# Performance work log

Hardware: AMD Instinct MI355X
Metric: run time of the kernel (lower is better)

The kernel has to match this reference:

```python
import jax, jax.numpy as jnp
import numpy as np

H, ND, RD, VD = 16, 128, 64, 128  # heads, nope/rope/v head dims
EPS = 1e-6


def rmsnorm(x, g):
    return x * jax.lax.rsqrt(jnp.mean(x * x, axis=-1, keepdims=True) + EPS) * g


def apply_rope(x, cos, sin):
    # x: [B,T,h,D]; cos/sin: [1,T,1,D/2]; interleaved pair rotation
    x1, x2 = x[..., 0::2], x[..., 1::2]
    o1 = x1 * cos - x2 * sin
    o2 = x1 * sin + x2 * cos
    return jnp.stack([o1, o2], axis=-1).reshape(x.shape)


def setup_inputs() -> dict:
    key = jax.random.key(0)
    ks = jax.random.split(key, 10)
    B, T, D = 2, 2048, 2048
    QR, KVR = 1536, 512
    s = 0.02
    return {
        "x": jax.random.normal(ks[0], (B, T, D), jnp.float32),
        "w_cq": jax.random.normal(ks[1], (D, QR), jnp.float32) * s,
        "g_q": jnp.ones((QR,), jnp.float32),
        "w_ckv": jax.random.normal(ks[2], (D, KVR), jnp.float32) * s,
        "g_kv": jnp.ones((KVR,), jnp.float32),
        "w_dq_nope": jax.random.normal(ks[3], (QR, H * ND), jnp.float32) * s,
        "w_dq_rope": jax.random.normal(ks[4], (QR, H * RD), jnp.float32) * s,
        "w_dk_nope": jax.random.normal(ks[5], (KVR, H * ND), jnp.float32) * s,
        "w_dv": jax.random.normal(ks[6], (KVR, H * VD), jnp.float32) * s,
        "w_k_rope": jax.random.normal(ks[7], (D, RD), jnp.float32) * s,
        "w_out": jax.random.normal(ks[8], (H * VD, D), jnp.float32) * s,
    }


def reference(x, w_cq, g_q, w_ckv, g_kv, w_dq_nope, w_dq_rope,
              w_dk_nope, w_dv, w_k_rope, w_out):
    B, T, D = x.shape
    # low-rank latents + RMSNorm
    q_lat = rmsnorm(x @ w_cq, g_q)          # [B,T,QR]
    kv_lat = rmsnorm(x @ w_ckv, g_kv)        # [B,T,KVR]
    q_nope = (q_lat @ w_dq_nope).reshape(B, T, H, ND)
    q_rope = (q_lat @ w_dq_rope).reshape(B, T, H, RD)
    k_nope = (kv_lat @ w_dk_nope).reshape(B, T, H, ND)
    v = (kv_lat @ w_dv).reshape(B, T, H, VD)
    k_rope = (x @ w_k_rope).reshape(B, T, 1, RD)  # shared across heads
    # RoPE (start_pos = 0, no past_kv)
    pos = jnp.arange(T, dtype=jnp.float32)
    inv_freq = 1.0 / (10000.0 ** (jnp.arange(0, RD, 2, dtype=jnp.float32) / RD))
    ang = pos[:, None] * inv_freq[None, :]               # [T, RD/2]
    cos = jnp.cos(ang)[None, :, None, :]
    sin = jnp.sin(ang)[None, :, None, :]
    q_rope = apply_rope(q_rope, cos, sin)
    k_rope = apply_rope(k_rope, cos, sin)
    k_rope = jnp.broadcast_to(k_rope, (B, T, H, RD))
    q = jnp.concatenate([q_nope, q_rope], axis=-1).transpose(0, 2, 1, 3)  # [B,H,T,ND+RD]
    k = jnp.concatenate([k_nope, k_rope], axis=-1).transpose(0, 2, 1, 3)
    v_t = v.transpose(0, 2, 1, 3)                                        # [B,H,T,VD]
    # causal SDPA, scale = 1/sqrt(head_dim)
    scale = 1.0 / jnp.sqrt(jnp.asarray(ND + RD, jnp.float32))
    scores = jnp.einsum('bhqd,bhkd->bhqk', q, k) * scale
    causal = jnp.tril(jnp.ones((T, T), dtype=bool))
    scores = jnp.where(causal[None, None], scores, -jnp.inf)
    attn = jax.nn.softmax(scores, axis=-1)
    out = jnp.einsum('bhqk,bhkd->bhqd', attn, v_t)
    out = out.transpose(0, 2, 1, 3).reshape(B, T, H * VD) @ w_out        # [B,T,D]
    return out, k, v_t
```

## Files before the change

kernel.cpp:

```cpp
#include <hip/hip_runtime.h>
#include <cstdint>
#include <cstddef>

typedef _Float16 HT;
typedef _Float16 h8 __attribute__((ext_vector_type(8)));
typedef _Float16 h4 __attribute__((ext_vector_type(4)));
typedef float f32x4 __attribute__((ext_vector_type(4)));

constexpr int Tn  = 2048;
constexpr int Dm  = 2048;
constexpr int Hh  = 16;
constexpr int RDc = 64;
constexpr int QRc = 1536;
constexpr int KVRc= 512;
constexpr int BT  = 4096;

#define VWAIT(N) asm volatile("s_waitcnt vmcnt(" #N ")" ::: "memory")
#define SBAR()   __builtin_amdgcn_s_barrier()

__device__ __forceinline__ f32x4 mfma16(h8 a, h8 b, f32x4 c) {
    return __builtin_amdgcn_mfma_f32_16x16x32_f16(a, b, c, 0, 0, 0);
}
__device__ __forceinline__ void gload_lds16(const void* g, void* l) {
    __builtin_amdgcn_global_load_lds(
        (const __attribute__((address_space(1))) unsigned int*)g,
        (__attribute__((address_space(3))) unsigned int*)l, 16, 0, 0);
}

__global__ __launch_bounds__(256)
void cstab_kernel(float2* __restrict__ cs)
{
    const int idx = blockIdx.x * 256 + threadIdx.x;
    const int t = idx >> 5, i = idx & 31;
    const float ang = (float)t * exp2f(-(float)i * (13.287712379549449f / 32.f));
    cs[idx] = make_float2(cosf(ang), sinf(ang));
}

__global__ __launch_bounds__(256)
void wtrans_kernel(const float* __restrict__ src, HT* __restrict__ dst,
                   int K, int N)
{
    __shared__ float Ts[64][65];
    const int k0 = blockIdx.y * 64, n0 = blockIdx.x * 64;
    const int tid = threadIdx.x;
    {
        const int r = tid >> 2, c0 = (tid & 3) * 16;
        const float* s = src + (size_t)(k0 + r) * N + n0 + c0;
        #pragma unroll
        for (int j = 0; j < 4; j++)
            *reinterpret_cast<f32x4*>(&Ts[r][c0 + j * 4]) = *reinterpret_cast<const f32x4*>(s + j * 4);
    }
    __syncthreads();
    {
        const int c = tid >> 2, kq = (tid & 3) * 16;
        h8 o0, o1;
        #pragma unroll
        for (int j = 0; j < 8; j++) { o0[j] = (HT)Ts[kq + j][c]; o1[j] = (HT)Ts[kq + 8 + j][c]; }
        HT* d = dst + (size_t)(n0 + c) * K + k0 + kq;
        *reinterpret_cast<h8*>(d)     = o0;
        *reinterpret_cast<h8*>(d + 8) = o1;
    }
}

__global__ __launch_bounds__(256)
void convx_kernel(const float* __restrict__ x, HT* __restrict__ x16)
{
    const size_t i = ((size_t)blockIdx.x * 256 + threadIdx.x) * 8;
    f32x4 a = *reinterpret_cast<const f32x4*>(x + i);
    f32x4 b = *reinterpret_cast<const f32x4*>(x + i + 4);
    h8 v;
    #pragma unroll
    for (int j = 0; j < 4; j++) { v[j] = (HT)a[j]; v[4 + j] = (HT)b[j]; }
    *reinterpret_cast<h8*>(x16 + i) = v;
}

template<int EPI>
__global__ __launch_bounds__(256)
void gemm16d(const HT* __restrict__ A, const HT* __restrict__ Bt, const int K,
             HT* __restrict__ o1, HT* __restrict__ o2, HT* __restrict__ o3,
             float* __restrict__ f1, float* __restrict__ f2,
             const float2* __restrict__ cstab)
{
    __shared__ HT As[2][4096];
    __shared__ HT Bs[2][4096];

    const int tid  = threadIdx.x;
    const int lane = tid & 63;
    const int l15  = lane & 15, l4 = lane >> 4;
    const int w    = tid >> 6;
    const int wr   = w >> 1, wc = w & 1;
    const int m0   = blockIdx.y * 128;
    const int n0   = blockIdx.x * 128;

    f32x4 acc[4][4] = {};
    const int nk = K >> 5;

#define GSTAGE(as_, bs_, kt_) do {                                             \
    _Pragma("unroll")                                                          \
    for (int i_ = 0; i_ < 2; i_++) {                                           \
        const int row_ = (w * 2 + i_) * 16 + (lane >> 2);                      \
        gload_lds16(A  + (size_t)(m0 + row_) * K + (kt_) + (lane & 3) * 8,     \
                    (as_) + (w * 2 + i_) * 512);                               \
        gload_lds16(Bt + (size_t)(n0 + row_) * K + (kt_) + (lane & 3) * 8,     \
                    (bs_) + (w * 2 + i_) * 512);                               \
    } } while (0)

    GSTAGE(As[0], Bs[0], 0);

    for (int kt = 0; kt < nk; kt++) {
        HT* as = As[kt & 1];
        HT* bs = Bs[kt & 1];
        if (kt + 1 < nk) {
            GSTAGE(As[(kt + 1) & 1], Bs[(kt + 1) & 1], (kt + 1) * 32);
            VWAIT(4);
        } else {
            VWAIT(0);
        }
        SBAR();

        h8 af[4], bf[4];
        #pragma unroll
        for (int f = 0; f < 4; f++)
            af[f] = *reinterpret_cast<const h8*>(&as[(wr * 64 + f * 16 + l15) * 32 + l4 * 8]);
        #pragma unroll
        for (int g = 0; g < 4; g++)
            bf[g] = *reinterpret_cast<const h8*>(&bs[(wc * 64 + g * 16 + l15) * 32 + l4 * 8]);
        #pragma unroll
        for (int f = 0; f < 4; f++)
            #pragma unroll
            for (int g = 0; g < 4; g++)
                acc[f][g] = mfma16(af[f], bf[g], acc[f][g]);
        SBAR();
    }
#undef GSTAGE

    #pragma unroll
    for (int f = 0; f < 4; f++) {
        #pragma unroll
        for (int g = 0; g < 4; g++) {
            const int row = m0 + wr * 64 + f * 16 + l4 * 4;
            const int col = n0 + wc * 64 + g * 16 + l15;
            if constexpr (EPI == 3) {
                #pragma unroll
                for (int r = 0; r < 4; r++)
                    f1[(size_t)(row + r) * 2048 + col] = acc[f][g][r];
            } else if constexpr (EPI == 0) {
                if (col < 1536) {
                    #pragma unroll
                    for (int r = 0; r < 4; r++)
                        o1[(size_t)(row + r) * 1536 + col] = (HT)acc[f][g][r];
                } else if (col < 2048) {
                    #pragma unroll
                    for (int r = 0; r < 4; r++)
                        o2[(size_t)(row + r) * 512 + (col - 1536)] = (HT)acc[f][g][r];
                } else if (col < 2112) {
                    const int cc = col - 2048;
                    const int i = cc >> 1;
                    const bool odd = cc & 1;
                    #pragma unroll
                    for (int r = 0; r < 4; r++) {
                        const int t = (row + r) & (Tn - 1);
                        const float2 cs = cstab[t * 32 + i];
                        const float v = acc[f][g][r];
                        const float p = __shfl_xor(v, 1);
                        const float ov = odd ? p * cs.y + v * cs.x : v * cs.x - p * cs.y;
                        o3[(size_t)(row + r) * 64 + cc] = (HT)ov;
                    }
                }
            } else if constexpr (EPI == 1) {
                if (col < 2048) {
                    #pragma unroll
                    for (int r = 0; r < 4; r++)
                        o1[(size_t)(row + r) * 2048 + col] = (HT)acc[f][g][r];
                } else {
                    const int cc = col - 2048;
                    const int i = (cc & 63) >> 1;
                    const bool odd = cc & 1;
                    #pragma unroll
                    for (int r = 0; r < 4; r++) {
                        const int t = (row + r) & (Tn - 1);
                        const float2 cs = cstab[t * 32 + i];
                        const float v = acc[f][g][r];
                        const float p = __shfl_xor(v, 1);
                        const float ov = odd ? p * cs.y + v * cs.x : v * cs.x - p * cs.y;
                        o2[(size_t)(row + r) * 1024 + cc] = (HT)ov;
                    }
                }
            } else {
                if (col < 2048) {
                    const int h = col >> 7, d = col & 127;
                    #pragma unroll
                    for (int r = 0; r < 4; r++) {
                        const int rw = row + r;
                        const int b = rw >> 11, t = rw & (Tn - 1);
                        o1[(size_t)rw * 2048 + col] = (HT)acc[f][g][r];
                        f1[((size_t)(b * Hh + h) * Tn + t) * 192 + d] = acc[f][g][r];
                    }
                } else {
                    const int c2 = col - 2048;
                    const int h = c2 >> 7, d = c2 & 127;
                    const int b = row >> 11, t0 = row & (Tn - 1);
                    h4 pk;
                    #pragma unroll
                    for (int r = 0; r < 4; r++) {
                        f2[((size_t)(b * Hh + h) * Tn + t0 + r) * 128 + d] = acc[f][g][r];
                        pk[r] = (HT)acc[f][g][r];
                    }
                    *reinterpret_cast<h4*>(&o3[((size_t)(b * Hh + h) * 128 + d) * Tn + t0]) = pk;
                }
            }
        }
    }
}

__global__ __launch_bounds__(256)
void kropebc_kernel(const HT* __restrict__ kr16, float* __restrict__ out_k)
{
    const int idx = blockIdx.x * 256 + threadIdx.x;
    const int j4 = (idx & 15) * 4;
    const int t  = (idx >> 4) & (Tn - 1);
    const int b  = idx >> 15;
    h4 v = *reinterpret_cast<const h4*>(&kr16[((size_t)(b * Tn + t)) * 64 + j4]);
    f32x4 f;
    #pragma unroll
    for (int r = 0; r < 4; r++) f[r] = (float)v[r];
    #pragma unroll
    for (int h = 0; h < Hh; h++)
        *reinterpret_cast<f32x4*>(&out_k[((size_t)(b * Hh + h) * Tn + t) * 192 + 128 + j4]) = f;
}

__global__ __launch_bounds__(256)
void rmsnorm_kernel(HT* __restrict__ X, const float* __restrict__ g, int N)
{
    const int row = blockIdx.x;
    HT* x = X + (size_t)row * N;
    float ss = 0.f;
    for (int i = threadIdx.x * 8; i < N; i += 2048) {
        h8 v = *reinterpret_cast<const h8*>(&x[i]);
        #pragma unroll
        for (int j = 0; j < 8; j++) { float f = (float)v[j]; ss += f * f; }
    }
    #pragma unroll
    for (int sh = 32; sh >= 1; sh >>= 1) ss += __shfl_xor(ss, sh);
    __shared__ float red[4];
    if ((threadIdx.x & 63) == 0) red[threadIdx.x >> 6] = ss;
    __syncthreads();
    const float tot = red[0] + red[1] + red[2] + red[3];
    const float scale = rsqrtf(tot / (float)N + 1e-6f);
    for (int i = threadIdx.x * 8; i < N; i += 2048) {
        h8 v = *reinterpret_cast<const h8*>(&x[i]);
        f32x4 g0 = *reinterpret_cast<const f32x4*>(&g[i]);
        f32x4 g1 = *reinterpret_cast<const f32x4*>(&g[i + 4]);
        #pragma unroll
        for (int j = 0; j < 4; j++) { v[j]   = (HT)((float)v[j]   * scale * g0[j]);
                                      v[4+j] = (HT)((float)v[4+j] * scale * g1[j]); }
        *reinterpret_cast<h8*>(&x[i]) = v;
    }
}

__global__ __launch_bounds__(256)
void attn6_kernel(const HT* __restrict__ qn, const HT* __restrict__ qr,
                  const HT* __restrict__ kn, const HT* __restrict__ kr16,
                  const HT* __restrict__ vt, HT* __restrict__ ao)
{
    __shared__ HT Ks_n[64 * 128];
    __shared__ HT Vs[128 * 64];
    __shared__ HT Ps[4][16][72];

    const int tid  = threadIdx.x;
    const int lane = tid & 63;
    const int l15  = lane & 15, l4 = lane >> 4;
    const int w    = tid >> 6;

    const int bid  = blockIdx.x;
    const int tile = 31 - (bid >> 5);
    const int h    = bid & 15;
    const int b    = (bid >> 4) & 1;

    const size_t bT = (size_t)b * Tn;
    const HT* vt_h = vt + ((size_t)(b * Hh + h) * 128) * Tn;
    const HT* krb  = kr16 + bT * 64;

    const int qw = tile * 64 + 16 * w;

    h8 aq[6];
    {
        const size_t rq = bT + qw + l15;
        const HT* pn = qn + rq * 2048 + h * 128 + l4 * 8;
        #pragma unroll
        for (int f = 0; f < 4; f++) aq[f] = *reinterpret_cast<const h8*>(pn + f * 32);
        const HT* pr = qr + rq * 1024 + h * 64 + l4 * 8;
        aq[4] = *reinterpret_cast<const h8*>(pr);
        aq[5] = *reinterpret_cast<const h8*>(pr + 32);
    }

    f32x4 o[8] = {};
    float m_i[4] = {-1e30f, -1e30f, -1e30f, -1e30f};
    float l_i[4] = {0.f, 0.f, 0.f, 0.f};

    const int nkb = tile + 1;
    for (int kb64 = 0; kb64 < nkb; kb64++) {
        const int kb = kb64 * 64;
        __syncthreads();
        #pragma unroll
        for (int j = 0; j < 4; j++) {
            const int r = (w * 4 + j) * 4 + l4;
            const int cl = (l15 & 8) | ((l15 & 7) ^ (r & 7));
            gload_lds16(kn + (bT + kb + r) * 2048 + h * 128 + cl * 8,
                        &Ks_n[(w * 4 + j) * 512]);
        }
        #pragma unroll
        for (int j = 0; j < 4; j++) {
            const int d = (w * 4 + j) * 8 + (lane >> 3);
            const int cl = (lane & 7) ^ (d & 7);
            gload_lds16(vt_h + (size_t)d * Tn + kb + cl * 8,
                        &Vs[(w * 4 + j) * 512]);
        }
        __syncthreads();

        if (kb <= qw + 15) {
            f32x4 s[4] = {};
            __builtin_amdgcn_s_setprio(1);
            #pragma unroll
            for (int c = 0; c < 4; c++) {
                const int kr = c * 16 + l15;
                const HT* rp = krb + (size_t)(kb + kr) * 64 + l4 * 8;
                const h8 br0 = *reinterpret_cast<const h8*>(rp);
                const h8 br1 = *reinterpret_cast<const h8*>(rp + 32);
                const int sw = (kr & 7) << 4;
                const char* kbase = (const char*)Ks_n + kr * 256;
                #pragma unroll
                for (int f = 0; f < 4; f++)
                    s[c] = mfma16(aq[f], *(const h8*)(kbase + ((f * 64 + l4 * 16) ^ sw)), s[c]);
                s[c] = mfma16(aq[4], br0, s[c]);
                s[c] = mfma16(aq[5], br1, s[c]);
            }
            __builtin_amdgcn_s_setprio(0);
            const float scl = 0.07216878364870323f;
            float al[4];
            #pragma unroll
            for (int r = 0; r < 4; r++) {
                const int qrow = qw + l4 * 4 + r;
                float a[4];
                #pragma unroll
                for (int c = 0; c < 4; c++)
                    a[c] = (kb + c * 16 + l15 <= qrow) ? s[c][r] * scl : -1e30f;
                float mx = fmaxf(fmaxf(a[0], a[1]), fmaxf(a[2], a[3]));
                #pragma unroll
                for (int sh = 1; sh < 16; sh <<= 1) mx = fmaxf(mx, __shfl_xor(mx, sh));
                const float mn = fmaxf(m_i[r], mx);
                const float alpha = __expf(m_i[r] - mn);
                m_i[r] = mn;
                float rs = 0.f;
                #pragma unroll
                for (int c = 0; c < 4; c++) {
                    const float e = __expf(a[c] - mn);
                    rs += e;
                    Ps[w][l4 * 4 + r][c * 16 + l15] = (HT)e;
                }
                #pragma unroll
                for (int sh = 1; sh < 16; sh <<= 1) rs += __shfl_xor(rs, sh);
                l_i[r] = l_i[r] * alpha + rs;
                al[r] = alpha;
            }
            #pragma unroll
            for (int g = 0; g < 8; g++)
                #pragma unroll
                for (int r = 0; r < 4; r++) o[g][r] *= al[r];

            const h8 ap0 = *reinterpret_cast<const h8*>(&Ps[w][l15][l4 * 8]);
            const h8 ap1 = *reinterpret_cast<const h8*>(&Ps[w][l15][32 + l4 * 8]);

            __builtin_amdgcn_s_setprio(1);
            #pragma unroll
            for (int g = 0; g < 8; g++) {
                const int d = g * 16 + l15;
                const int sw = (d & 7) << 4;
                const char* vbase = (const char*)Vs + d * 128;
                h8 v0 = *(const h8*)(vbase + ((l4 * 16) ^ sw));
                h8 v1 = *(const h8*)(vbase + ((64 + l4 * 16) ^ sw));
                o[g] = mfma16(ap0, v0, o[g]);
                o[g] = mfma16(ap1, v1, o[g]);
            }
            __builtin_amdgcn_s_setprio(0);
        }
    }

    const size_t orow = bT + qw + l4 * 4;
    #pragma unroll
    for (int r = 0; r < 4; r++) {
        const float inv = 1.0f / l_i[r];
        HT* dst = ao + (orow + r) * 2048 + h * 128 + l15;
        #pragma unroll
        for (int g = 0; g < 8; g++) dst[g * 16] = (HT)(o[g][r] * inv);
    }
}

extern "C" void kernel_launch(void* const* d_in, const int* in_sizes, int n_in,
                              void* d_out, int out_size, void* d_ws, size_t ws_size,
                              hipStream_t stream)
{
    const float* x     = (const float*)d_in[0];
    const float* w_cq  = (const float*)d_in[1];
    const float* g_q   = (const float*)d_in[2];
    const float* w_ckv = (const float*)d_in[3];
    const float* g_kv  = (const float*)d_in[4];
    const float* w_dqn = (const float*)d_in[5];
    const float* w_dqr = (const float*)d_in[6];
    const float* w_dkn = (const float*)d_in[7];
    const float* w_dv  = (const float*)d_in[8];
    const float* w_kr  = (const float*)d_in[9];
    const float* w_out = (const float*)d_in[10];

    char* ws = (char*)d_ws;
    HT* cqT   = (HT*)(ws + 0);
    HT* ckvT  = (HT*)(ws + 6291456);
    HT* krT   = (HT*)(ws + 8388608);
    HT* dqnT  = (HT*)(ws + 8912896);
    HT* dqrT  = (HT*)(ws + 15204352);
    HT* dknT  = (HT*)(ws + 18350080);
    HT* dvT   = (HT*)(ws + 20447232);
    HT* outT  = (HT*)(ws + 22544384);
    HT* cq    = (HT*)(ws + 30932992);
    HT* ckv   = (HT*)(ws + 43515904);
    HT* qn    = (HT*)(ws + 47710208);
    HT* qr    = (HT*)(ws + 64487424);
    HT* kn    = (HT*)(ws + 72876032);
    HT* kr16  = (HT*)(ws + 89653248);
    HT* vt    = (HT*)(ws + 0);
    HT* x16   = qn;
    HT* ao    = qn;

    float* out_o = (float*)d_out;
    float* out_k = out_o + (size_t)BT * Dm;
    float* out_v = out_k + (size_t)2 * Hh * Tn * 192;
    float2* cstab = (float2*)out_v;

    const dim3 blk(256);

    cstab_kernel<<<dim3(256), blk, 0, stream>>>(cstab);
    wtrans_kernel<<<dim3(QRc/64,  Dm/64), blk, 0, stream>>>(w_cq,  cqT,  Dm,  QRc);
    wtrans_kernel<<<dim3(KVRc/64, Dm/64), blk, 0, stream>>>(w_ckv, ckvT, Dm,  KVRc);
    wtrans_kernel<<<dim3(RDc/64,  Dm/64), blk, 0, stream>>>(w_kr,  krT,  Dm,  RDc);
    wtrans_kernel<<<dim3(Dm/64, QRc/64),  blk, 0, stream>>>(w_dqn, dqnT, QRc, Dm);
    wtrans_kernel<<<dim3((Hh*RDc)/64, QRc/64), blk, 0, stream>>>(w_dqr, dqrT, QRc, Hh*RDc);
    wtrans_kernel<<<dim3(Dm/64, KVRc/64), blk, 0, stream>>>(w_dkn, dknT, KVRc, Dm);
    wtrans_kernel<<<dim3(Dm/64, KVRc/64), blk, 0, stream>>>(w_dv,  dvT,  KVRc, Dm);
    wtrans_kernel<<<dim3(Dm/64, Dm/64),   blk, 0, stream>>>(w_out, outT, Dm,  Dm);

    convx_kernel<<<dim3(4096), blk, 0, stream>>>(x, x16);

    gemm16d<0><<<dim3(17, BT/128), blk, 0, stream>>>(x16, cqT, Dm,
        cq, ckv, kr16, nullptr, nullptr, cstab);
    kropebc_kernel<<<dim3(256), blk, 0, stream>>>(kr16, out_k);

    rmsnorm_kernel<<<dim3(BT), blk, 0, stream>>>(cq,  g_q,  QRc);
    rmsnorm_kernel<<<dim3(BT), blk, 0, stream>>>(ckv, g_kv, KVRc);

    gemm16d<1><<<dim3(24, BT/128), blk, 0, stream>>>(cq, dqnT, QRc,
        qn, qr, nullptr, nullptr, nullptr, cstab);
    gemm16d<2><<<dim3(32, BT/128), blk, 0, stream>>>(ckv, dknT, KVRc,
        kn, nullptr, vt, out_k, out_v, nullptr);

    attn6_kernel<<<dim3(1024), blk, 0, stream>>>(qn, qr, kn, kr16, vt, ao);

    gemm16d<3><<<dim3(16, BT/128), blk, 0, stream>>>(ao, outT, Dm,
        nullptr, nullptr, nullptr, out_o, nullptr, nullptr);
}
```

Before: 382.7 us.

## Pair causal query tiles in attention, swizzle GEMM LDS, batch small launches

The attention kernel now gives each block two query tiles, j and 31-j. This balances causal work across 512 blocks and reuses each loaded K/V tile for both query sets. The GEMM LDS staging gains an XOR chunk swizzle on both the global-to-LDS writes and the fragment reads to cut bank conflicts. The eight weight-transpose launches are merged into one segmented kernel, and the two RMSNorm launches into one 2D grid, to reduce launch overhead. The paired attention doubles the per-wave accumulator registers and sets launch bounds of 2 blocks, which may limit occupancy.

```diff
diff --git a/kernel.cpp b/kernel.cpp
--- a/kernel.cpp
+++ b/kernel.cpp
@@ -36,12 +36,25 @@
     cs[idx] = make_float2(cosf(ang), sinf(ang));
 }
 
+struct WT8 {
+    const float* s[8];
+    HT* d[8];
+    int K[8], N[8], start[8];
+};
+
 __global__ __launch_bounds__(256)
-void wtrans_kernel(const float* __restrict__ src, HT* __restrict__ dst,
-                   int K, int N)
+void wtrans8_kernel(WT8 p)
 {
     __shared__ float Ts[64][65];
-    const int k0 = blockIdx.y * 64, n0 = blockIdx.x * 64;
+    int seg = 0;
+    #pragma unroll
+    for (int i = 1; i < 8; i++) if ((int)blockIdx.x >= p.start[i]) seg = i;
+    const float* src = p.s[seg];
+    HT* dst = p.d[seg];
+    const int K = p.K[seg], N = p.N[seg];
+    const int bx = blockIdx.x - p.start[seg];
+    const int nx = N >> 6;
+    const int n0 = (bx % nx) * 64, k0 = (bx / nx) * 64;
     const int tid = threadIdx.x;
     {
         const int r = tid >> 2, c0 = (tid & 3) * 16;
@@ -95,17 +108,21 @@
     f32x4 acc[4][4] = {};
     const int nk = K >> 5;
 
+    const int schunk = ((lane & 3) ^ ((lane >> 2) & 3) ^ ((lane >> 4) & 3)) * 8;
+
 #define GSTAGE(as_, bs_, kt_) do {                                             \
     _Pragma("unroll")                                                          \
     for (int i_ = 0; i_ < 2; i_++) {                                           \
         const int row_ = (w * 2 + i_) * 16 + (lane >> 2);                      \
-        gload_lds16(A  + (size_t)(m0 + row_) * K + (kt_) + (lane & 3) * 8,     \
+        gload_lds16(A  + (size_t)(m0 + row_) * K + (kt_) + schunk,             \
                     (as_) + (w * 2 + i_) * 512);                               \
-        gload_lds16(Bt + (size_t)(n0 + row_) * K + (kt_) + (lane & 3) * 8,     \
+        gload_lds16(Bt + (size_t)(n0 + row_) * K + (kt_) + schunk,             \
                     (bs_) + (w * 2 + i_) * 512);                               \
     } } while (0)
 
     GSTAGE(As[0], Bs[0], 0);
+
+    const int sl = (l4 ^ (l15 & 3) ^ ((l15 >> 2) & 3)) * 8;
 
     for (int kt = 0; kt < nk; kt++) {
         HT* as = As[kt & 1];
@@ -121,10 +138,10 @@
         h8 af[4], bf[4];
         #pragma unroll
         for (int f = 0; f < 4; f++)
-            af[f] = *reinterpret_cast<const h8*>(&as[(wr * 64 + f * 16 + l15) * 32 + l4 * 8]);
+            af[f] = *reinterpret_cast<const h8*>(&as[(wr * 64 + f * 16 + l15) * 32 + sl]);
         #pragma unroll
         for (int g = 0; g < 4; g++)
-            bf[g] = *reinterpret_cast<const h8*>(&bs[(wc * 64 + g * 16 + l15) * 32 + l4 * 8]);
+            bf[g] = *reinterpret_cast<const h8*>(&bs[(wc * 64 + g * 16 + l15) * 32 + sl]);
         #pragma unroll
         for (int f = 0; f < 4; f++)
             #pragma unroll
@@ -230,8 +247,13 @@
 }
 
 __global__ __launch_bounds__(256)
-void rmsnorm_kernel(HT* __restrict__ X, const float* __restrict__ g, int N)
-{
+void rmsnorm2_kernel(HT* __restrict__ Xa, const float* __restrict__ ga,
+                     HT* __restrict__ Xb, const float* __restrict__ gb)
+{
+    const int which = blockIdx.y;
+    HT* X = which ? Xb : Xa;
+    const float* g = which ? gb : ga;
+    const int N = which ? 512 : 1536;
     const int row = blockIdx.x;
     HT* x = X + (size_t)row * N;
     float ss = 0.f;
@@ -258,141 +280,186 @@
     }
 }
 
-__global__ __launch_bounds__(256)
-void attn6_kernel(const HT* __restrict__ qn, const HT* __restrict__ qr,
+__global__ __launch_bounds__(256, 2)
+void attn7_kernel(const HT* __restrict__ qn, const HT* __restrict__ qr,
                   const HT* __restrict__ kn, const HT* __restrict__ kr16,
                   const HT* __restrict__ vt, HT* __restrict__ ao)
 {
     __shared__ HT Ks_n[64 * 128];
     __shared__ HT Vs[128 * 64];
-    __shared__ HT Ps[4][16][72];
+    __shared__ HT Ps[4][32][72];
 
     const int tid  = threadIdx.x;
     const int lane = tid & 63;
     const int l15  = lane & 15, l4 = lane >> 4;
     const int w    = tid >> 6;
 
-    const int bid  = blockIdx.x;
-    const int tile = 31 - (bid >> 5);
-    const int h    = bid & 15;
-    const int b    = (bid >> 4) & 1;
+    const int bid = blockIdx.x;
+    const int j   = bid >> 5;
+    const int h   = bid & 15;
+    const int b   = (bid >> 4) & 1;
+    const int thi = 31 - j;
 
     const size_t bT = (size_t)b * Tn;
     const HT* vt_h = vt + ((size_t)(b * Hh + h) * 128) * Tn;
     const HT* krb  = kr16 + bT * 64;
 
-    const int qw = tile * 64 + 16 * w;
-
-    h8 aq[6];
+    const int qw0 = j   * 64 + w * 16;
+    const int qw1 = thi * 64 + w * 16;
+
+    h8 aq0[6], aq1[6];
     {
-        const size_t rq = bT + qw + l15;
-        const HT* pn = qn + rq * 2048 + h * 128 + l4 * 8;
-        #pragma unroll
-        for (int f = 0; f < 4; f++) aq[f] = *reinterpret_cast<const h8*>(pn + f * 32);
-        const HT* pr = qr + rq * 1024 + h * 64 + l4 * 8;
-        aq[4] = *reinterpret_cast<const h8*>(pr);
-        aq[5] = *reinterpret_cast<const h8*>(pr + 32);
-    }
-
-    f32x4 o[8] = {};
-    float m_i[4] = {-1e30f, -1e30f, -1e30f, -1e30f};
-    float l_i[4] = {0.f, 0.f, 0.f, 0.f};
-
-    const int nkb = tile + 1;
+        const size_t rq0 = bT + qw0 + l15;
+        const HT* pn = qn + rq0 * 2048 + h * 128 + l4 * 8;
+        #pragma unroll
+        for (int f = 0; f < 4; f++) aq0[f] = *reinterpret_cast<const h8*>(pn + f * 32);
+        const HT* pr = qr + rq0 * 1024 + h * 64 + l4 * 8;
+        aq0[4] = *reinterpret_cast<const h8*>(pr);
+        aq0[5] = *reinterpret_cast<const h8*>(pr + 32);
+        const size_t rq1 = bT + qw1 + l15;
+        const HT* pn1 = qn + rq1 * 2048 + h * 128 + l4 * 8;
+        #pragma unroll
+        for (int f = 0; f < 4; f++) aq1[f] = *reinterpret_cast<const h8*>(pn1 + f * 32);
+        const HT* pr1 = qr + rq1 * 1024 + h * 64 + l4 * 8;
+        aq1[4] = *reinterpret_cast<const h8*>(pr1);
+        aq1[5] = *reinterpret_cast<const h8*>(pr1 + 32);
+    }
+
+    f32x4 o0[8] = {}, o1[8] = {};
+    float m0v[4] = {-1e30f, -1e30f, -1e30f, -1e30f};
+    float m1v[4] = {-1e30f, -1e30f, -1e30f, -1e30f};
+    float l0v[4] = {0.f, 0.f, 0.f, 0.f};
+    float l1v[4] = {0.f, 0.f, 0.f, 0.f};
+
+    const float scl = 0.07216878364870323f;
+
+#define SOFTMAX(sv, mv, lv, ov, qwx, prow)                                      \
+{                                                                               \
+    float al_[4];                                                               \
+    _Pragma("unroll")                                                           \
+    for (int r = 0; r < 4; r++) {                                               \
+        const int qrow = (qwx) + l4 * 4 + r;                                    \
+        float a_[4];                                                            \
+        _Pragma("unroll")                                                       \
+        for (int c = 0; c < 4; c++)                                             \
+            a_[c] = (kb + c * 16 + l15 <= qrow) ? sv[c][r] * scl : -1e30f;      \
+        float mx = fmaxf(fmaxf(a_[0], a_[1]), fmaxf(a_[2], a_[3]));             \
+        _Pragma("unroll")                                                       \
+        for (int sh = 1; sh < 16; sh <<= 1) mx = fmaxf(mx, __shfl_xor(mx, sh)); \
+        const float mn = fmaxf(mv[r], mx);                                      \
+        const float alpha = __expf(mv[r] - mn);                                 \
+        mv[r] = mn;                                                             \
+        float rs = 0.f;                                                         \
+        _Pragma("unroll")                                                       \
+        for (int c = 0; c < 4; c++) {                                           \
+            const float e = __expf(a_[c] - mn);                                 \
+            rs += e;                                                            \
+            Ps[w][(prow) + l4 * 4 + r][c * 16 + l15] = (HT)e;                   \
+        }                                                                       \
+        _Pragma("unroll")                                                       \
+        for (int sh = 1; sh < 16; sh <<= 1) rs += __shfl_xor(rs, sh);           \
+        lv[r] = lv[r] * alpha + rs;                                             \
+        al_[r] = alpha;                                                         \
+    }                                                                           \
+    _Pragma("unroll")                                                           \
+    for (int g = 0; g < 8; g++)                                                 \
+        _Pragma("unroll")                                                       \
+        for (int r = 0; r < 4; r++) ov[g][r] *= al_[r];                         \
+}
+
+#define KBODY(ACT0)                                                             \
+{                                                                               \
+    f32x4 s0[4] = {}, s1[4] = {};                                               \
+    __builtin_amdgcn_s_setprio(1);                                              \
+    _Pragma("unroll")                                                           \
+    for (int c = 0; c < 4; c++) {                                               \
+        const int kr = c * 16 + l15;                                            \
+        const HT* rp = krb + (size_t)(kb + kr) * 64 + l4 * 8;                   \
+        const h8 br0 = *reinterpret_cast<const h8*>(rp);                        \
+        const h8 br1 = *reinterpret_cast<const h8*>(rp + 32);                   \
+        const int sw = (kr & 7) << 4;                                           \
+        const char* kbase = (const char*)Ks_n + kr * 256;                       \
+        _Pragma("unroll")                                                       \
+        for (int f = 0; f < 4; f++) {                                           \
+            const h8 kf = *(const h8*)(kbase + ((f * 64 + l4 * 16) ^ sw));      \
+            s1[c] = mfma16(aq1[f], kf, s1[c]);                                  \
+            if (ACT0) s0[c] = mfma16(aq0[f], kf, s0[c]);                        \
+        }                                                                       \
+        s1[c] = mfma16(aq1[4], br0, s1[c]);                                     \
+        s1[c] = mfma16(aq1[5], br1, s1[c]);                                     \
+        if (ACT0) { s0[c] = mfma16(aq0[4], br0, s0[c]);                         \
+                    s0[c] = mfma16(aq0[5], br1, s0[c]); }                       \
+    }                                                                           \
+    __builtin_amdgcn_s_setprio(0);                                              \
+    SOFTMAX(s1, m1v, l1v, o1, qw1, 16);                                         \
+    if (ACT0) SOFTMAX(s0, m0v, l0v, o0, qw0, 0);                                \
+    const h8 ap10 = *reinterpret_cast<const h8*>(&Ps[w][16 + l15][l4 * 8]);     \
+    const h8 ap11 = *reinterpret_cast<const h8*>(&Ps[w][16 + l15][32 + l4 * 8]);\
+    h8 ap00 = ap10, ap01 = ap11;                                                \
+    if (ACT0) {                                                                 \
+        ap00 = *reinterpret_cast<const h8*>(&Ps[w][l15][l4 * 8]);               \
+        ap01 = *reinterpret_cast<const h8*>(&Ps[w][l15][32 + l4 * 8]);          \
+    }                                                                           \
+    __builtin_amdgcn_s_setprio(1);                                              \
+    _Pragma("unroll")                                                           \
+    for (int g = 0; g < 8; g++) {                                               \
+        const int d = g * 16 + l15;                                             \
+        const int sw = (d & 7) << 4;                                            \
+        const char* vbase = (const char*)Vs + d * 128;                          \
+        const h8 v0 = *(const h8*)(vbase + ((l4 * 16) ^ sw));                   \
+        const h8 v1 = *(const h8*)(vbase + ((64 + l4 * 16) ^ sw));              \
+        o1[g] = mfma16(ap10, v0, o1[g]);                                        \
+        o1[g] = mfma16(ap11, v1, o1[g]);                                        \
+        if (ACT0) { o0[g] = mfma16(ap00, v0, o0[g]);                            \
+                    o0[g] = mfma16(ap01, v1, o0[g]); }                          \
+    }                                                                           \
+    __builtin_amdgcn_s_setprio(0);                                              \
+}
+
+    const int nkb = thi + 1;
     for (int kb64 = 0; kb64 < nkb; kb64++) {
         const int kb = kb64 * 64;
         __syncthreads();
         #pragma unroll
-        for (int j = 0; j < 4; j++) {
-            const int r = (w * 4 + j) * 4 + l4;
+        for (int jj = 0; jj < 4; jj++) {
+            const int r = (w * 4 + jj) * 4 + l4;
             const int cl = (l15 & 8) | ((l15 & 7) ^ (r & 7));
             gload_lds16(kn + (bT + kb + r) * 2048 + h * 128 + cl * 8,
-                        &Ks_n[(w * 4 + j) * 512]);
-        }
-        #pragma unroll
-        for (int j = 0; j < 4; j++) {
-            const int d = (w * 4 + j) * 8 + (lane >> 3);
+                        &Ks_n[(w * 4 + jj) * 512]);
+        }
+        #pragma unroll
+        for (int jj = 0; jj < 4; jj++) {
+            const int d = (w * 4 + jj) * 8 + (lane >> 3);
             const int cl = (lane & 7) ^ (d & 7);
             gload_lds16(vt_h + (size_t)d * Tn + kb + cl * 8,
-                        &Vs[(w * 4 + j) * 512]);
+                        &Vs[(w * 4 + jj) * 512]);
         }
         __syncthreads();
 
-        if (kb <= qw + 15) {
-            f32x4 s[4] = {};
-            __builtin_amdgcn_s_setprio(1);
+        if (kb <= qw0 + 15) KBODY(1) else KBODY(0)
+    }
+#undef KBODY
+#undef SOFTMAX
+
+    {
+        const size_t orow = bT + qw1 + l4 * 4;
+        #pragma unroll
+        for (int r = 0; r < 4; r++) {
+            const float inv = 1.0f / l1v[r];
+            HT* dst = ao + (orow + r) * 2048 + h * 128 + l15;
             #pragma unroll
-            for (int c = 0; c < 4; c++) {
-                const int kr = c * 16 + l15;
-                const HT* rp = krb + (size_t)(kb + kr) * 64 + l4 * 8;
-                const h8 br0 = *reinterpret_cast<const h8*>(rp);
-                const h8 br1 = *reinterpret_cast<const h8*>(rp + 32);
-                const int sw = (kr & 7) << 4;
-                const char* kbase = (const char*)Ks_n + kr * 256;
-                #pragma unroll
-                for (int f = 0; f < 4; f++)
-                    s[c] = mfma16(aq[f], *(const h8*)(kbase + ((f * 64 + l4 * 16) ^ sw)), s[c]);
-                s[c] = mfma16(aq[4], br0, s[c]);
-                s[c] = mfma16(aq[5], br1, s[c]);
-            }
-            __builtin_amdgcn_s_setprio(0);
-            const float scl = 0.07216878364870323f;
-            float al[4];
+            for (int g = 0; g < 8; g++) dst[g * 16] = (HT)(o1[g][r] * inv);
+        }
+    }
+    {
+        const size_t orow = bT + qw0 + l4 * 4;
+        #pragma unroll
+        for (int r = 0; r < 4; r++) {
+            const float inv = 1.0f / l0v[r];
+            HT* dst = ao + (orow + r) * 2048 + h * 128 + l15;
             #pragma unroll
-            for (int r = 0; r < 4; r++) {
-                const int qrow = qw + l4 * 4 + r;
-                float a[4];
-                #pragma unroll
-                for (int c = 0; c < 4; c++)
-                    a[c] = (kb + c * 16 + l15 <= qrow) ? s[c][r] * scl : -1e30f;
-                float mx = fmaxf(fmaxf(a[0], a[1]), fmaxf(a[2], a[3]));
-                #pragma unroll
-                for (int sh = 1; sh < 16; sh <<= 1) mx = fmaxf(mx, __shfl_xor(mx, sh));
-                const float mn = fmaxf(m_i[r], mx);
-                const float alpha = __expf(m_i[r] - mn);
-                m_i[r] = mn;
-                float rs = 0.f;
-                #pragma unroll
-                for (int c = 0; c < 4; c++) {
-                    const float e = __expf(a[c] - mn);
-                    rs += e;
-                    Ps[w][l4 * 4 + r][c * 16 + l15] = (HT)e;
-                }
-                #pragma unroll
-                for (int sh = 1; sh < 16; sh <<= 1) rs += __shfl_xor(rs, sh);
-                l_i[r] = l_i[r] * alpha + rs;
-                al[r] = alpha;
-            }
-            #pragma unroll
-            for (int g = 0; g < 8; g++)
-                #pragma unroll
-                for (int r = 0; r < 4; r++) o[g][r] *= al[r];
-
-            const h8 ap0 = *reinterpret_cast<const h8*>(&Ps[w][l15][l4 * 8]);
-            const h8 ap1 = *reinterpret_cast<const h8*>(&Ps[w][l15][32 + l4 * 8]);
-
-            __builtin_amdgcn_s_setprio(1);
-            #pragma unroll
-            for (int g = 0; g < 8; g++) {
-                const int d = g * 16 + l15;
-                const int sw = (d & 7) << 4;
-                const char* vbase = (const char*)Vs + d * 128;
-                h8 v0 = *(const h8*)(vbase + ((l4 * 16) ^ sw));
-                h8 v1 = *(const h8*)(vbase + ((64 + l4 * 16) ^ sw));
-                o[g] = mfma16(ap0, v0, o[g]);
-                o[g] = mfma16(ap1, v1, o[g]);
-            }
-            __builtin_amdgcn_s_setprio(0);
-        }
-    }
-
-    const size_t orow = bT + qw + l4 * 4;
-    #pragma unroll
-    for (int r = 0; r < 4; r++) {
-        const float inv = 1.0f / l_i[r];
-        HT* dst = ao + (orow + r) * 2048 + h * 128 + l15;
-        #pragma unroll
-        for (int g = 0; g < 8; g++) dst[g * 16] = (HT)(o[g][r] * inv);
+            for (int g = 0; g < 8; g++) dst[g * 16] = (HT)(o0[g][r] * inv);
+        }
     }
 }
 
@@ -439,14 +506,24 @@
     const dim3 blk(256);
 
     cstab_kernel<<<dim3(256), blk, 0, stream>>>(cstab);
-    wtrans_kernel<<<dim3(QRc/64,  Dm/64), blk, 0, stream>>>(w_cq,  cqT,  Dm,  QRc);
-    wtrans_kernel<<<dim3(KVRc/64, Dm/64), blk, 0, stream>>>(w_ckv, ckvT, Dm,  KVRc);
-    wtrans_kernel<<<dim3(RDc/64,  Dm/64), blk, 0, stream>>>(w_kr,  krT,  Dm,  RDc);
-    wtrans_kernel<<<dim3(Dm/64, QRc/64),  blk, 0, stream>>>(w_dqn, dqnT, QRc, Dm);
-    wtrans_kernel<<<dim3((Hh*RDc)/64, QRc/64), blk, 0, stream>>>(w_dqr, dqrT, QRc, Hh*RDc);
-    wtrans_kernel<<<dim3(Dm/64, KVRc/64), blk, 0, stream>>>(w_dkn, dknT, KVRc, Dm);
-    wtrans_kernel<<<dim3(Dm/64, KVRc/64), blk, 0, stream>>>(w_dv,  dvT,  KVRc, Dm);
-    wtrans_kernel<<<dim3(Dm/64, Dm/64),   blk, 0, stream>>>(w_out, outT, Dm,  Dm);
+
+    WT8 wt;
+    wt.s[0]=w_cq;  wt.d[0]=cqT;  wt.K[0]=2048; wt.N[0]=1536;
+    wt.s[1]=w_ckv; wt.d[1]=ckvT; wt.K[1]=2048; wt.N[1]=512;
+    wt.s[2]=w_kr;  wt.d[2]=krT;  wt.K[2]=2048; wt.N[2]=64;
+    wt.s[3]=w_dqn; wt.d[3]=dqnT; wt.K[3]=1536; wt.N[3]=2048;
+    wt.s[4]=w_dqr; wt.d[4]=dqrT; wt.K[4]=1536; wt.N[4]=1024;
+    wt.s[5]=w_dkn; wt.d[5]=dknT; wt.K[5]=512;  wt.N[5]=2048;
+    wt.s[6]=w_dv;  wt.d[6]=dvT;  wt.K[6]=512;  wt.N[6]=2048;
+    wt.s[7]=w_out; wt.d[7]=outT; wt.K[7]=2048; wt.N[7]=2048;
+    {
+        int acc = 0;
+        for (int i = 0; i < 8; i++) {
+            wt.start[i] = acc;
+            acc += (wt.N[i] >> 6) * (wt.K[i] >> 6);
+        }
+        wtrans8_kernel<<<dim3(acc), blk, 0, stream>>>(wt);
+    }
 
     convx_kernel<<<dim3(4096), blk, 0, stream>>>(x, x16);
 
@@ -454,15 +531,14 @@
         cq, ckv, kr16, nullptr, nullptr, cstab);
     kropebc_kernel<<<dim3(256), blk, 0, stream>>>(kr16, out_k);
 
-    rmsnorm_kernel<<<dim3(BT), blk, 0, stream>>>(cq,  g_q,  QRc);
-    rmsnorm_kernel<<<dim3(BT), blk, 0, stream>>>(ckv, g_kv, KVRc);
+    rmsnorm2_kernel<<<dim3(BT, 2), blk, 0, stream>>>(cq, g_q, ckv, g_kv);
 
     gemm16d<1><<<dim3(24, BT/128), blk, 0, stream>>>(cq, dqnT, QRc,
         qn, qr, nullptr, nullptr, nullptr, cstab);
     gemm16d<2><<<dim3(32, BT/128), blk, 0, stream>>>(ckv, dknT, KVRc,
         kn, nullptr, vt, out_k, out_v, nullptr);
 
-    attn6_kernel<<<dim3(1024), blk, 0, stream>>>(qn, qr, kn, kr16, vt, ao);
+    attn7_kernel<<<dim3(512), blk, 0, stream>>>(qn, qr, kn, kr16, vt, ao);
 
     gemm16d<3><<<dim3(16, BT/128), blk, 0, stream>>>(ao, outT, Dm,
         nullptr, nullptr, nullptr, out_o, nullptr, nullptr);
```

Result: faster. 357.8 us (-6.5%).

## Rewrite attention with 32x32 MFMA, paired causal tiles, and batch small kernel launches

Applied to the files above, without the earlier changes.

Attention is rewritten around 32x32x16 MFMA with P kept in registers and exchanged by cross-lane shuffles instead of an LDS round trip. Each block pairs a short and a long causal query tile to balance work, and the rescale is skipped lazily when the running max grows by less than a threshold. The scale is folded into Q with exp2. Separately, the GEMM LDS layout gets an XOR swizzle to avoid bank conflicts, the eight weight-transpose launches are merged into one, and the two RMSNorm launches are merged into one. The cost is higher register pressure and more complex indexing in the attention kernel.

```diff
diff --git a/kernel.cpp b/kernel.cpp
--- a/kernel.cpp
+++ b/kernel.cpp
@@ -6,6 +6,7 @@
 typedef _Float16 h8 __attribute__((ext_vector_type(8)));
 typedef _Float16 h4 __attribute__((ext_vector_type(4)));
 typedef float f32x4 __attribute__((ext_vector_type(4)));
+typedef float f32x16 __attribute__((ext_vector_type(16)));
 
 constexpr int Tn  = 2048;
 constexpr int Dm  = 2048;
@@ -21,11 +22,19 @@
 __device__ __forceinline__ f32x4 mfma16(h8 a, h8 b, f32x4 c) {
     return __builtin_amdgcn_mfma_f32_16x16x32_f16(a, b, c, 0, 0, 0);
 }
+__device__ __forceinline__ f32x16 mfma32(h8 a, h8 b, f32x16 c) {
+    return __builtin_amdgcn_mfma_f32_32x32x16_f16(a, b, c, 0, 0, 0);
+}
 __device__ __forceinline__ void gload_lds16(const void* g, void* l) {
     __builtin_amdgcn_global_load_lds(
         (const __attribute__((address_space(1))) unsigned int*)g,
         (__attribute__((address_space(3))) unsigned int*)l, 16, 0, 0);
 }
+__device__ __forceinline__ unsigned pkf16(float a, float b) {
+    union { _Float16 h[2]; unsigned u; } t;
+    t.h[0] = (_Float16)a; t.h[1] = (_Float16)b;
+    return t.u;
+}
 
 __global__ __launch_bounds__(256)
 void cstab_kernel(float2* __restrict__ cs)
@@ -36,12 +45,25 @@
     cs[idx] = make_float2(cosf(ang), sinf(ang));
 }
 
-__global__ __launch_bounds__(256)
-void wtrans_kernel(const float* __restrict__ src, HT* __restrict__ dst,
-                   int K, int N)
+struct WT8 {
+    const float* s[8];
+    HT* d[8];
+    int K[8], N[8], start[8];
+};
+
+__global__ __launch_bounds__(256)
+void wtrans8_kernel(WT8 p)
 {
     __shared__ float Ts[64][65];
-    const int k0 = blockIdx.y * 64, n0 = blockIdx.x * 64;
+    int seg = 0;
+    #pragma unroll
+    for (int i = 1; i < 8; i++) if ((int)blockIdx.x >= p.start[i]) seg = i;
+    const float* src = p.s[seg];
+    HT* dst = p.d[seg];
+    const int K = p.K[seg], N = p.N[seg];
+    const int bx = blockIdx.x - p.start[seg];
+    const int nx = N >> 6;
+    const int n0 = (bx % nx) * 64, k0 = (bx / nx) * 64;
     const int tid = threadIdx.x;
     {
         const int r = tid >> 2, c0 = (tid & 3) * 16;
@@ -95,17 +117,21 @@
     f32x4 acc[4][4] = {};
     const int nk = K >> 5;
 
+    const int schunk = ((lane & 3) ^ ((lane >> 2) & 3) ^ ((lane >> 4) & 3)) * 8;
+
 #define GSTAGE(as_, bs_, kt_) do {                                             \
     _Pragma("unroll")                                                          \
     for (int i_ = 0; i_ < 2; i_++) {                                           \
         const int row_ = (w * 2 + i_) * 16 + (lane >> 2);                      \
-        gload_lds16(A  + (size_t)(m0 + row_) * K + (kt_) + (lane & 3) * 8,     \
+        gload_lds16(A  + (size_t)(m0 + row_) * K + (kt_) + schunk,             \
                     (as_) + (w * 2 + i_) * 512);                               \
-        gload_lds16(Bt + (size_t)(n0 + row_) * K + (kt_) + (lane & 3) * 8,     \
+        gload_lds16(Bt + (size_t)(n0 + row_) * K + (kt_) + schunk,             \
                     (bs_) + (w * 2 + i_) * 512);                               \
     } } while (0)
 
     GSTAGE(As[0], Bs[0], 0);
+
+    const int sl = (l4 ^ (l15 & 3) ^ ((l15 >> 2) & 3)) * 8;
 
     for (int kt = 0; kt < nk; kt++) {
         HT* as = As[kt & 1];
@@ -121,10 +147,10 @@
         h8 af[4], bf[4];
         #pragma unroll
         for (int f = 0; f < 4; f++)
-            af[f] = *reinterpret_cast<const h8*>(&as[(wr * 64 + f * 16 + l15) * 32 + l4 * 8]);
+            af[f] = *reinterpret_cast<const h8*>(&as[(wr * 64 + f * 16 + l15) * 32 + sl]);
         #pragma unroll
         for (int g = 0; g < 4; g++)
-            bf[g] = *reinterpret_cast<const h8*>(&bs[(wc * 64 + g * 16 + l15) * 32 + l4 * 8]);
+            bf[g] = *reinterpret_cast<const h8*>(&bs[(wc * 64 + g * 16 + l15) * 32 + sl]);
         #pragma unroll
         for (int f = 0; f < 4; f++)
             #pragma unroll
@@ -230,8 +256,13 @@
 }
 
 __global__ __launch_bounds__(256)
-void rmsnorm_kernel(HT* __restrict__ X, const float* __restrict__ g, int N)
-{
+void rmsnorm2_kernel(HT* __restrict__ Xa, const float* __restrict__ ga,
+                     HT* __restrict__ Xb, const float* __restrict__ gb)
+{
+    const int which = blockIdx.y;
+    HT* X = which ? Xb : Xa;
+    const float* g = which ? gb : ga;
+    const int N = which ? 512 : 1536;
     const int row = blockIdx.x;
     HT* x = X + (size_t)row * N;
     float ss = 0.f;
@@ -259,140 +290,172 @@
 }
 
 __global__ __launch_bounds__(256)
-void attn6_kernel(const HT* __restrict__ qn, const HT* __restrict__ qr,
+void attn8_kernel(const HT* __restrict__ qn, const HT* __restrict__ qr,
                   const HT* __restrict__ kn, const HT* __restrict__ kr16,
                   const HT* __restrict__ vt, HT* __restrict__ ao)
 {
-    __shared__ HT Ks_n[64 * 128];
+    __shared__ HT Ks[64 * 128];
     __shared__ HT Vs[128 * 64];
-    __shared__ HT Ps[4][16][72];
 
     const int tid  = threadIdx.x;
     const int lane = tid & 63;
-    const int l15  = lane & 15, l4 = lane >> 4;
+    const int l31  = lane & 31;
+    const int hi   = lane >> 5;
     const int w    = tid >> 6;
 
-    const int bid  = blockIdx.x;
-    const int tile = 31 - (bid >> 5);
-    const int h    = bid & 15;
-    const int b    = (bid >> 4) & 1;
+    const int bid = blockIdx.x;
+    const int wid = (bid & 7) * 64 + (bid >> 3);
+    const int j   = wid & 15;
+    const int hb  = wid >> 4;
+    const int h   = hb >> 1;
+    const int b   = hb & 1;
 
     const size_t bT = (size_t)b * Tn;
     const HT* vt_h = vt + ((size_t)(b * Hh + h) * 128) * Tn;
     const HT* krb  = kr16 + bT * 64;
 
-    const int qw = tile * 64 + 16 * w;
-
-    h8 aq[6];
+    const int mytile = (w < 2) ? j : (31 - j);
+    const int qw   = mytile * 64 + (w & 1) * 32;
+    const int qabs = qw + l31;
+
+    h8 bq[12];
     {
-        const size_t rq = bT + qw + l15;
-        const HT* pn = qn + rq * 2048 + h * 128 + l4 * 8;
-        #pragma unroll
-        for (int f = 0; f < 4; f++) aq[f] = *reinterpret_cast<const h8*>(pn + f * 32);
-        const HT* pr = qr + rq * 1024 + h * 64 + l4 * 8;
-        aq[4] = *reinterpret_cast<const h8*>(pr);
-        aq[5] = *reinterpret_cast<const h8*>(pr + 32);
-    }
-
-    f32x4 o[8] = {};
-    float m_i[4] = {-1e30f, -1e30f, -1e30f, -1e30f};
-    float l_i[4] = {0.f, 0.f, 0.f, 0.f};
-
-    const int nkb = tile + 1;
+        const HT sc = (HT)(0.07216878364870323f * 1.4426950408889634f);
+        const HT* pn = qn + (bT + qabs) * 2048 + h * 128 + hi * 8;
+        #pragma unroll
+        for (int s = 0; s < 8; s++) bq[s] = *reinterpret_cast<const h8*>(pn + s * 16) * sc;
+        const HT* pr = qr + (bT + qabs) * 1024 + h * 64 + hi * 8;
+        #pragma unroll
+        for (int s = 0; s < 4; s++) bq[8 + s] = *reinterpret_cast<const h8*>(pr + s * 16) * sc;
+    }
+
+    f32x16 O[4] = {};
+    float m_i = -1e30f, l_i = 0.f;
+
+    const int nkb = 32 - j;
     for (int kb64 = 0; kb64 < nkb; kb64++) {
         const int kb = kb64 * 64;
         __syncthreads();
         #pragma unroll
-        for (int j = 0; j < 4; j++) {
-            const int r = (w * 4 + j) * 4 + l4;
-            const int cl = (l15 & 8) | ((l15 & 7) ^ (r & 7));
+        for (int c = 0; c < 4; c++) {
+            const int r  = (w * 4 + c) * 4 + (lane >> 4);
+            const int cl = (lane & 15) ^ (r & 15);
             gload_lds16(kn + (bT + kb + r) * 2048 + h * 128 + cl * 8,
-                        &Ks_n[(w * 4 + j) * 512]);
-        }
-        #pragma unroll
-        for (int j = 0; j < 4; j++) {
-            const int d = (w * 4 + j) * 8 + (lane >> 3);
+                        &Ks[(w * 4 + c) * 512]);
+        }
+        #pragma unroll
+        for (int c = 0; c < 4; c++) {
+            const int d  = (w * 4 + c) * 8 + (lane >> 3);
             const int cl = (lane & 7) ^ (d & 7);
             gload_lds16(vt_h + (size_t)d * Tn + kb + cl * 8,
-                        &Vs[(w * 4 + j) * 512]);
+                        &Vs[(w * 4 + c) * 512]);
         }
         __syncthreads();
 
-        if (kb <= qw + 15) {
-            f32x4 s[4] = {};
-            __builtin_amdgcn_s_setprio(1);
+        if (kb <= qw + 31) {
             #pragma unroll
-            for (int c = 0; c < 4; c++) {
-                const int kr = c * 16 + l15;
-                const HT* rp = krb + (size_t)(kb + kr) * 64 + l4 * 8;
-                const h8 br0 = *reinterpret_cast<const h8*>(rp);
-                const h8 br1 = *reinterpret_cast<const h8*>(rp + 32);
-                const int sw = (kr & 7) << 4;
-                const char* kbase = (const char*)Ks_n + kr * 256;
-                #pragma unroll
-                for (int f = 0; f < 4; f++)
-                    s[c] = mfma16(aq[f], *(const h8*)(kbase + ((f * 64 + l4 * 16) ^ sw)), s[c]);
-                s[c] = mfma16(aq[4], br0, s[c]);
-                s[c] = mfma16(aq[5], br1, s[c]);
+            for (int grp = 0; grp < 2; grp++) {
+                const int krow = grp * 32 + l31;
+                f32x16 sA = {}, sB = {};
+                __builtin_amdgcn_s_setprio(1);
+                #pragma unroll
+                for (int st = 0; st < 4; st++) {
+                    const int chA = (st * 2 + hi) ^ (krow & 15);
+                    const int chB = ((st + 4) * 2 + hi) ^ (krow & 15);
+                    sA = mfma32(*reinterpret_cast<const h8*>(&Ks[krow * 128 + chA * 8]), bq[st], sA);
+                    sB = mfma32(*reinterpret_cast<const h8*>(&Ks[krow * 128 + chB * 8]), bq[st + 4], sB);
+                }
+                {
+                    const HT* rp = krb + (size_t)(kb + krow) * 64 + hi * 8;
+                    sA = mfma32(*reinterpret_cast<const h8*>(rp),      bq[8],  sA);
+                    sB = mfma32(*reinterpret_cast<const h8*>(rp + 16), bq[9],  sB);
+                    sA = mfma32(*reinterpret_cast<const h8*>(rp + 32), bq[10], sA);
+                    sB = mfma32(*reinterpret_cast<const h8*>(rp + 48), bq[11], sB);
+                }
+                __builtin_amdgcn_s_setprio(0);
+
+                float p[16];
+                float mx = -1e30f;
+                #pragma unroll
+                for (int r = 0; r < 16; r++) {
+                    const int kl  = (r & 3) + 8 * (r >> 2) + 4 * hi;
+                    const int kab = kb + grp * 32 + kl;
+                    const float sv = sA[r] + sB[r];
+                    p[r] = (kab <= qabs) ? sv : -1e30f;
+                    mx = fmaxf(mx, p[r]);
+                }
+                mx = fmaxf(mx, __shfl_xor(mx, 32));
+                if (!__all(mx <= m_i + 8.f)) {
+                    const float mn = fmaxf(m_i, mx);
+                    const float alpha = __builtin_exp2f(m_i - mn);
+                    m_i = mn;
+                    l_i *= alpha;
+                    float av[16];
+                    #pragma unroll
+                    for (int r = 0; r < 16; r++) {
+                        const int ql = (r & 3) + 8 * (r >> 2) + 4 * hi;
+                        av[r] = __shfl(alpha, ql);
+                    }
+                    #pragma unroll
+                    for (int db = 0; db < 4; db++)
+                        #pragma unroll
+                        for (int r = 0; r < 16; r++) O[db][r] *= av[r];
+                }
+                float rs = 0.f;
+                #pragma unroll
+                for (int r = 0; r < 16; r++) {
+                    p[r] = __builtin_exp2f(p[r] - m_i);
+                    rs += p[r];
+                }
+                l_i += rs + __shfl_xor(rs, 32);
+
+                unsigned u[8], sw[8];
+                #pragma unroll
+                for (int bb = 0; bb < 4; bb++) {
+                    u[2 * bb]     = pkf16(p[4 * bb],     p[4 * bb + 1]);
+                    u[2 * bb + 1] = pkf16(p[4 * bb + 2], p[4 * bb + 3]);
+                }
+                #pragma unroll
+                for (int i = 0; i < 8; i++) sw[i] = (unsigned)__shfl_xor((int)u[i], 32);
+
+                __builtin_amdgcn_s_setprio(1);
+                #pragma unroll
+                for (int t = 0; t < 2; t++) {
+                    const int bb = 2 * t + hi;
+                    union { unsigned uu[4]; h8 v; } pa;
+                    pa.uu[0] = hi ? sw[2 * bb]     : u[2 * bb];
+                    pa.uu[1] = hi ? sw[2 * bb + 1] : u[2 * bb + 1];
+                    pa.uu[2] = hi ? u[2 * bb]      : sw[2 * bb];
+                    pa.uu[3] = hi ? u[2 * bb + 1]  : sw[2 * bb + 1];
+                    const int ch = grp * 4 + 2 * t + hi;
+                    #pragma unroll
+                    for (int db = 0; db < 4; db++) {
+                        const int d = db * 32 + l31;
+                        const h8 vf = *reinterpret_cast<const h8*>(&Vs[d * 64 + ((ch ^ (d & 7)) * 8)]);
+                        O[db] = mfma32(pa.v, vf, O[db]);
+                    }
+                }
+                __builtin_amdgcn_s_setprio(0);
             }
-            __builtin_amdgcn_s_setprio(0);
-            const float scl = 0.07216878364870323f;
-            float al[4];
-            #pragma unroll
-            for (int r = 0; r < 4; r++) {
-                const int qrow = qw + l4 * 4 + r;
-                float a[4];
-                #pragma unroll
-                for (int c = 0; c < 4; c++)
-                    a[c] = (kb + c * 16 + l15 <= qrow) ? s[c][r] * scl : -1e30f;
-                float mx = fmaxf(fmaxf(a[0], a[1]), fmaxf(a[2], a[3]));
-                #pragma unroll
-                for (int sh = 1; sh < 16; sh <<= 1) mx = fmaxf(mx, __shfl_xor(mx, sh));
-                const float mn = fmaxf(m_i[r], mx);
-                const float alpha = __expf(m_i[r] - mn);
-                m_i[r] = mn;
-                float rs = 0.f;
-                #pragma unroll
-                for (int c = 0; c < 4; c++) {
-                    const float e = __expf(a[c] - mn);
-                    rs += e;
-                    Ps[w][l4 * 4 + r][c * 16 + l15] = (HT)e;
-                }
-                #pragma unroll
-                for (int sh = 1; sh < 16; sh <<= 1) rs += __shfl_xor(rs, sh);
-                l_i[r] = l_i[r] * alpha + rs;
-                al[r] = alpha;
-            }
-            #pragma unroll
-            for (int g = 0; g < 8; g++)
-                #pragma unroll
-                for (int r = 0; r < 4; r++) o[g][r] *= al[r];
-
-            const h8 ap0 = *reinterpret_cast<const h8*>(&Ps[w][l15][l4 * 8]);
-            const h8 ap1 = *reinterpret_cast<const h8*>(&Ps[w][l15][32 + l4 * 8]);
-
-            __builtin_amdgcn_s_setprio(1);
-            #pragma unroll
-            for (int g = 0; g < 8; g++) {
-                const int d = g * 16 + l15;
-                const int sw = (d & 7) << 4;
-                const char* vbase = (const char*)Vs + d * 128;
-                h8 v0 = *(const h8*)(vbase + ((l4 * 16) ^ sw));
-                h8 v1 = *(const h8*)(vbase + ((64 + l4 * 16) ^ sw));
-                o[g] = mfma16(ap0, v0, o[g]);
-                o[g] = mfma16(ap1, v1, o[g]);
-            }
-            __builtin_amdgcn_s_setprio(0);
-        }
-    }
-
-    const size_t orow = bT + qw + l4 * 4;
-    #pragma unroll
-    for (int r = 0; r < 4; r++) {
-        const float inv = 1.0f / l_i[r];
-        HT* dst = ao + (orow + r) * 2048 + h * 128 + l15;
-        #pragma unroll
-        for (int g = 0; g < 8; g++) dst[g * 16] = (HT)(o[g][r] * inv);
+        }
+    }
+
+    float iv[16];
+    {
+        const float inv = 1.0f / l_i;
+        #pragma unroll
+        for (int r = 0; r < 16; r++) {
+            const int ql = (r & 3) + 8 * (r >> 2) + 4 * hi;
+            iv[r] = __shfl(inv, ql);
+        }
+    }
+    #pragma unroll
+    for (int db = 0; db < 4; db++) {
+        #pragma unroll
+        for (int r = 0; r < 16; r++) {
+            const int ql = (r & 3) + 8 * (r >> 2) + 4 * hi;
+            ao[(bT + qw + ql) * 2048 + h * 128 + db * 32 + l31] = (HT)(O[db][r] * iv[r]);
+        }
     }
 }
 
@@ -439,14 +502,24 @@
     const dim3 blk(256);
 
     cstab_kernel<<<dim3(256), blk, 0, stream>>>(cstab);
-    wtrans_kernel<<<dim3(QRc/64,  Dm/64), blk, 0, stream>>>(w_cq,  cqT,  Dm,  QRc);
-    wtrans_kernel<<<dim3(KVRc/64, Dm/64), blk, 0, stream>>>(w_ckv, ckvT, Dm,  KVRc);
-    wtrans_kernel<<<dim3(RDc/64,  Dm/64), blk, 0, stream>>>(w_kr,  krT,  Dm,  RDc);
-    wtrans_kernel<<<dim3(Dm/64, QRc/64),  blk, 0, stream>>>(w_dqn, dqnT, QRc, Dm);
-    wtrans_kernel<<<dim3((Hh*RDc)/64, QRc/64), blk, 0, stream>>>(w_dqr, dqrT, QRc, Hh*RDc);
-    wtrans_kernel<<<dim3(Dm/64, KVRc/64), blk, 0, stream>>>(w_dkn, dknT, KVRc, Dm);
-    wtrans_kernel<<<dim3(Dm/64, KVRc/64), blk, 0, stream>>>(w_dv,  dvT,  KVRc, Dm);
-    wtrans_kernel<<<dim3(Dm/64, Dm/64),   blk, 0, stream>>>(w_out, outT, Dm,  Dm);
+
+    WT8 wt;
+    wt.s[0]=w_cq;  wt.d[0]=cqT;  wt.K[0]=2048; wt.N[0]=1536;
+    wt.s[1]=w_ckv; wt.d[1]=ckvT; wt.K[1]=2048; wt.N[1]=512;
+    wt.s[2]=w_kr;  wt.d[2]=krT;  wt.K[2]=2048; wt.N[2]=64;
+    wt.s[3]=w_dqn; wt.d[3]=dqnT; wt.K[3]=1536; wt.N[3]=2048;
+    wt.s[4]=w_dqr; wt.d[4]=dqrT; wt.K[4]=1536; wt.N[4]=1024;
+    wt.s[5]=w_dkn; wt.d[5]=dknT; wt.K[5]=512;  wt.N[5]=2048;
+    wt.s[6]=w_dv;  wt.d[6]=dvT;  wt.K[6]=512;  wt.N[6]=2048;
+    wt.s[7]=w_out; wt.d[7]=outT; wt.K[7]=2048; wt.N[7]=2048;
+    {
+        int acc = 0;
+        for (int i = 0; i < 8; i++) {
+            wt.start[i] = acc;
+            acc += (wt.N[i] >> 6) * (wt.K[i] >> 6);
+        }
+        wtrans8_kernel<<<dim3(acc), blk, 0, stream>>>(wt);
+    }
 
     convx_kernel<<<dim3(4096), blk, 0, stream>>>(x, x16);
 
@@ -454,15 +527,14 @@
         cq, ckv, kr16, nullptr, nullptr, cstab);
     kropebc_kernel<<<dim3(256), blk, 0, stream>>>(kr16, out_k);
 
-    rmsnorm_kernel<<<dim3(BT), blk, 0, stream>>>(cq,  g_q,  QRc);
-    rmsnorm_kernel<<<dim3(BT), blk, 0, stream>>>(ckv, g_kv, KVRc);
+    rmsnorm2_kernel<<<dim3(BT, 2), blk, 0, stream>>>(cq, g_q, ckv, g_kv);
 
     gemm16d<1><<<dim3(24, BT/128), blk, 0, stream>>>(cq, dqnT, QRc,
         qn, qr, nullptr, nullptr, nullptr, cstab);
     gemm16d<2><<<dim3(32, BT/128), blk, 0, stream>>>(ckv, dknT, KVRc,
         kn, nullptr, vt, out_k, out_v, nullptr);
 
-    attn6_kernel<<<dim3(1024), blk, 0, stream>>>(qn, qr, kn, kr16, vt, ao);
+    attn8_kernel<<<dim3(512), blk, 0, stream>>>(qn, qr, kn, kr16, vt, ao);
 
     gemm16d<3><<<dim3(16, BT/128), blk, 0, stream>>>(ao, outT, Dm,
         nullptr, nullptr, nullptr, out_o, nullptr, nullptr);
```

Result: slower. 486.9 us (+27.2%).
